# Performance work log

Hardware: AMD Instinct MI355X
Metric: run time of the kernel (lower is better)

The kernel has to match this reference:

```python
import jax, jax.numpy as jnp
import numpy as np

B, T, NIN, H1, H2, E, A = 256, 128, 1024, 512, 512, 256, 16
EPS = 1e-5


def setup_inputs() -> dict:
    key = jax.random.key(0)
    ks = jax.random.split(key, 24)
    def lin(k, fan_in, fan_out):
        # weights stored [in, out]; y = x @ W + b (equivalent to torch Linear)
        s = 1.0 / np.sqrt(fan_in)
        kw, kb = jax.random.split(k)
        return (jax.random.uniform(kw, (fan_in, fan_out), jnp.float32, -s, s),
                jax.random.uniform(kb, (fan_out,), jnp.float32, -s, s))
    W1, b1 = lin(ks[0], NIN, H1)
    W2, b2 = lin(ks[1], H1, H2)
    W3, b3 = lin(ks[2], H2, E)
    Wih, bih = lin(ks[3], E, 3 * E)   # GRUCell input weights, gate order [r, z, n]
    Whh, bhh = lin(ks[4], E, 3 * E)   # GRUCell hidden weights
    Whe, bhe = lin(ks[5], E + A, E)   # hidden_encoder
    Wae, bae = lin(ks[6], A, A)       # action_encoder
    return {
        'obs': jax.random.normal(ks[7], (B, T, NIN), jnp.float32),
        'actions': jax.random.normal(ks[8], (B, T, A), jnp.float32),
        'W1': W1, 'b1': b1, 'g1': jnp.ones((H1,), jnp.float32), 'be1': jnp.zeros((H1,), jnp.float32),
        'W2': W2, 'b2': b2, 'g2': jnp.ones((H2,), jnp.float32), 'be2': jnp.zeros((H2,), jnp.float32),
        'W3': W3, 'b3': b3,
        'Wih': Wih, 'bih': bih, 'Whh': Whh, 'bhh': bhh,
        'Whe': Whe, 'bhe': bhe, 'Wae': Wae, 'bae': bae,
    }


def reference(obs, actions, W1, b1, g1, be1, W2, b2, g2, be2, W3, b3,
              Wih, bih, Whh, bhh, Whe, bhe, Wae, bae):
    def bn(x, g, b):  # BatchNorm1d, training mode (batch stats, biased var)
        mu = jnp.mean(x, axis=0)
        var = jnp.mean((x - mu) ** 2, axis=0)
        return g * (x - mu) / jnp.sqrt(var + EPS) + b

    def mlp(x):
        x = jax.nn.elu(bn(x @ W1 + b1, g1, be1))
        x = jax.nn.elu(bn(x @ W2 + b2, g2, be2))
        return x @ W3 + b3

    def gru(x, h):
        gi = x @ Wih + bih
        gh = h @ Whh + bhh
        ir, iz, inn = jnp.split(gi, 3, axis=1)
        hr, hz, hn = jnp.split(gh, 3, axis=1)
        r = jax.nn.sigmoid(ir + hr)
        z = jax.nn.sigmoid(iz + hz)
        n = jnp.tanh(inn + r * hn)
        return (1.0 - z) * n + z * h

    obs_t = jnp.swapaxes(obs, 0, 1)       # [T, B, NIN]
    act_t = jnp.swapaxes(actions, 0, 1)   # [T, B, A]
    h0 = jnp.zeros((obs.shape[0], E), jnp.float32)
    a0 = jnp.zeros((obs.shape[0], A), jnp.float32)

    def step(carry, xs):
        h, a_prev = carry
        o, a = xs
        h = jnp.concatenate([h, a_prev], axis=1) @ Whe + bhe
        a_prev = a @ Wae + bae
        h = gru(mlp(o), h)
        return (h, a_prev), None

    (h, _), _ = jax.lax.scan(step, (h0, a0), (obs_t, act_t))
    return h
```

## Files before the change

kernel.cpp:

```cpp
#include <hip/hip_runtime.h>
#include <math.h>
#include <stdint.h>

#define B_   256
#define T_   128
#define NIN_ 1024
#define H1_  512
#define E_   256
#define A_   16
#define MT_  (B_ * T_)

typedef unsigned short ushort_t;
typedef unsigned long long ull_t;
typedef __attribute__((ext_vector_type(8))) short   short8;
typedef __attribute__((ext_vector_type(8))) __bf16  bf16x8;
typedef __attribute__((ext_vector_type(4))) float   f32x4;

union frag8 { short8 s; bf16x8 b; };

__device__ __forceinline__ ushort_t f2bf(float f) {
  union { float f; unsigned u; } v; v.f = f;
  unsigned r = (v.u + 0x7FFFu + ((v.u >> 16) & 1u)) >> 16;
  return (ushort_t)r;
}

static constexpr size_t OFF_C0    = 0;
static constexpr size_t OFF_OBSB  = 0;
static constexpr size_t OFF_Y     = 134217728;
static constexpr size_t OFF_YG    = 134217728;
static constexpr size_t OFF_XG    = 167772160;
static constexpr size_t OFF_PENCB = 184549376;
static constexpr size_t OFF_XB    = 201326592;
static constexpr size_t OFF_INN   = 201326592;
static constexpr size_t OFF_AE    = 234881024;
static constexpr size_t OFF_W1T   = 236978176;
static constexpr size_t OFF_W2T   = 238026752;
static constexpr size_t OFF_W3T   = 238551040;
static constexpr size_t OFF_WIHT  = 239075328;
static constexpr size_t OFF_WHHT  = 239468544;
static constexpr size_t OFF_WCT   = 240123904;
static constexpr size_t OFF_BSUM  = 241172480;
static constexpr size_t OFF_FLAGS = 241176576;
static constexpr size_t OFF_HG    = 241238016;


__global__ __launch_bounds__(256) void cast_obs_k(const float* __restrict__ obs,
                                                  ushort_t* __restrict__ out) {
  int row_in = blockIdx.x;
  int b = row_in / T_, t = row_in - b * T_;
  const float4* s4 = (const float4*)(obs + (size_t)row_in * NIN_);
  float4 v = s4[threadIdx.x];
  ushort_t* d = out + (size_t)(t * B_ + b) * NIN_ + threadIdx.x * 4;
  d[0] = f2bf(v.x); d[1] = f2bf(v.y); d[2] = f2bf(v.z); d[3] = f2bf(v.w);
}

__global__ __launch_bounds__(256) void transpose_cast_k(const float* __restrict__ in,
                                                        ushort_t* __restrict__ out,
                                                        int R, int C) {
  __shared__ float tile[32][33];
  int c0 = blockIdx.x * 32, r0 = blockIdx.y * 32;
  int tx = threadIdx.x & 31, ty = threadIdx.x >> 5;
  for (int i = 0; i < 4; i++) {
    int r = r0 + ty * 4 + i;
    if (r < R && (c0 + tx) < C) tile[ty * 4 + i][tx] = in[(size_t)r * C + c0 + tx];
  }
  __syncthreads();
  for (int i = 0; i < 4; i++) {
    int c = c0 + ty * 4 + i, r = r0 + tx;
    if (c < C && r < R) out[(size_t)c * R + r] = f2bf(tile[tx][ty * 4 + i]);
  }
}

__global__ __launch_bounds__(256) void wct_a_k(const float* __restrict__ Whe,
                                               ushort_t* __restrict__ Wct) {
  int c = blockIdx.x, k = threadIdx.x;
  Wct[(size_t)c * 256 + k] = f2bf(Whe[(size_t)k * 256 + c]);
}

__global__ __launch_bounds__(256) void wct_b_k(const float* __restrict__ Whe,
                                               const float* __restrict__ Whh,
                                               ushort_t* __restrict__ Wct) {
  int c = blockIdx.x;
  int k = threadIdx.x;
  float acc = 0.f;
  for (int j = 0; j < 256; j++)
    acc += Whe[(size_t)k * 256 + j] * Whh[(size_t)j * 768 + c];
  Wct[(size_t)(256 + c) * 256 + k] = f2bf(acc);
}

__global__ void bsum_k(const float* __restrict__ bih, const float* __restrict__ bhh,
                       float* __restrict__ bs) {
  int i = blockIdx.x * 256 + threadIdx.x;
  if (i < 768) bs[i] = bih[i] + bhh[i];
}

__global__ void init_flags_k(unsigned* f) {
  if (threadIdx.x < 16) f[threadIdx.x * 32] = 0u;
}

__global__ __launch_bounds__(256) void ae_k(const float* __restrict__ actions,
                                            const float* __restrict__ Wae,
                                            const float* __restrict__ bae,
                                            float* __restrict__ AE) {
  int idx = blockIdx.x * 256 + threadIdx.x;
  int m = idx >> 4, k2 = idx & 15;
  int t = m >> 8, b = m & 255;
  const float* arow = actions + ((size_t)b * T_ + t) * A_;
  float acc = bae[k2];
  for (int k = 0; k < 16; k++) acc += arow[k] * Wae[k * 16 + k2];
  AE[(size_t)m * 16 + k2] = acc;
}

__global__ __launch_bounds__(256) void penc_k(const float* __restrict__ AE,
                                              const float* __restrict__ Whe,
                                              const float* __restrict__ bhe,
                                              float* __restrict__ C0,
                                              ushort_t* __restrict__ Pencb) {
  int m = blockIdx.x;
  int j = threadIdx.x;
  __shared__ float a[16];
  if (threadIdx.x < 16)
    a[threadIdx.x] = (m >= B_) ? AE[(size_t)(m - B_) * 16 + threadIdx.x] : 0.f;
  __syncthreads();
  float acc = bhe[j];
  if (m >= B_) {
    for (int k = 0; k < 16; k++) acc += a[k] * Whe[(size_t)(256 + k) * 256 + j];
  }
  C0[(size_t)m * 1024 + j] = acc;
  Pencb[(size_t)m * 256 + j] = f2bf(acc);
}

__global__ __launch_bounds__(256) void bn_elu_k(const float* __restrict__ Y,
                                                const float* __restrict__ g,
                                                const float* __restrict__ be,
                                                ushort_t* __restrict__ Xb) {
  int t = blockIdx.x, f = blockIdx.y * 256 + threadIdx.x;
  const float* base = Y + (size_t)t * B_ * H1_;
  float s = 0.f, ss = 0.f;
  for (int b = 0; b < B_; b++) {
    float v = base[(size_t)b * H1_ + f];
    s += v; ss += v * v;
  }
  float mu  = s * (1.f / B_);
  float var = ss * (1.f / B_) - mu * mu;
  float inv = 1.f / sqrtf(var + 1e-5f);
  float sc = g[f] * inv, sh = be[f] - mu * sc;
  ushort_t* ob = Xb + (size_t)t * B_ * H1_;
  for (int b = 0; b < B_; b++) {
    float v = base[(size_t)b * H1_ + f] * sc + sh;
    float e = v > 0.f ? v : (expf(v) - 1.f);
    ob[(size_t)b * H1_ + f] = f2bf(e);
  }
}

__global__ __launch_bounds__(256) void cast_k(const float* __restrict__ in,
                                              ushort_t* __restrict__ out, long n) {
  long i = (long)blockIdx.x * 256 + threadIdx.x;
  if (i < n) out[i] = f2bf(in[i]);
}

__global__ __launch_bounds__(256) void gemm_bt_k(const ushort_t* __restrict__ A, int lda,
                                                 const ushort_t* __restrict__ Bt, int ldb,
                                                 float* __restrict__ C, int ldc,
                                                 const float* __restrict__ bias,
                                                 int K, int accum) {
  __shared__ __align__(16) ushort_t As[128][40];
  __shared__ __align__(16) ushort_t Bs[128][40];
  int tid = threadIdx.x;
  int wave = tid >> 6, lane = tid & 63;
  int q = lane >> 4, l15 = lane & 15;
  int wr = wave >> 1, wc = wave & 1;
  int m0 = blockIdx.x * 128, n0 = blockIdx.y * 128;
  f32x4 acc[4][4] = {};
  int r = tid >> 1, sh = (tid & 1) * 16;
  const ushort_t* aSrc = A + (size_t)(m0 + r) * lda + sh;
  const ushort_t* bSrc = Bt + (size_t)(n0 + r) * ldb + sh;
  for (int k0 = 0; k0 < K; k0 += 32) {
    *(short8*)&As[r][sh]     = *(const short8*)(aSrc + k0);
    *(short8*)&As[r][sh + 8] = *(const short8*)(aSrc + k0 + 8);
    *(short8*)&Bs[r][sh]     = *(const short8*)(bSrc + k0);
    *(short8*)&Bs[r][sh + 8] = *(const short8*)(bSrc + k0 + 8);
    __syncthreads();
    frag8 af[4], bf[4];
#pragma unroll
    for (int i = 0; i < 4; i++) {
      af[i].s = *(const short8*)&As[wr * 64 + i * 16 + l15][q * 8];
      bf[i].s = *(const short8*)&Bs[wc * 64 + i * 16 + l15][q * 8];
    }
#pragma unroll
    for (int at = 0; at < 4; at++)
#pragma unroll
      for (int bt = 0; bt < 4; bt++)
        acc[at][bt] = __builtin_amdgcn_mfma_f32_16x16x32_bf16(af[at].b, bf[bt].b, acc[at][bt], 0, 0, 0);
    __syncthreads();
  }
#pragma unroll
  for (int at = 0; at < 4; at++)
#pragma unroll
    for (int bt = 0; bt < 4; bt++) {
      int mb = m0 + wr * 64 + at * 16 + q * 4;
      int n  = n0 + wc * 64 + bt * 16 + l15;
      float bv = bias ? bias[n] : 0.f;
#pragma unroll
      for (int i = 0; i < 4; i++) {
        size_t idx = (size_t)(mb + i) * ldc + n;
        float v = acc[at][bt][i] + bv;
        if (accum) v += C[idx];
        C[idx] = v;
      }
    }
}

__global__ __launch_bounds__(1024) void gru_cols_k(
    const ushort_t* __restrict__ Wct,
    const float* __restrict__ C0,
    const float* __restrict__ INN,
    ull_t* __restrict__ hG,
    unsigned* __restrict__ flags,
    float* __restrict__ outF) {
  __shared__ __align__(16) ushort_t Wb[256][264];
  __shared__ __align__(16) ushort_t h_lds[16][264];
  __shared__ float G[4][16][66];
  __shared__ unsigned go, lcnt;

  const int tid = threadIdx.x;
  const int w = tid >> 6, lane = tid & 63;
  const int q = lane >> 4, l15 = lane & 15;
  const int rg = blockIdx.x & 15, cg = blockIdx.x >> 4;
  const int r0 = rg * 16;
  const int g = w >> 2, j = w & 3;

  unsigned* flag = flags + rg * 32;

  if (tid == 0) { go = 0u; lcnt = 0u; }
  for (int d = tid; d < 16 * 264 / 2; d += 1024) ((unsigned*)h_lds)[d] = 0u;
  for (int i = tid; i < 256 * 32; i += 1024) {
    int rr = i >> 5, ss = i & 31;
    int srow = (rr >> 6) * 256 + cg * 64 + (rr & 63);
    *(short8*)&Wb[rr][ss * 8] = *(const short8*)(Wct + (size_t)srow * 256 + ss * 8);
  }
  __syncthreads();

  const int crow = w;
  const int ccol = lane;
  const int hg = cg * 64 + ccol;

  for (int t = 0; t < T_; t++) {
    const float* c0t  = C0  + ((size_t)t * B_ + r0) * 1024;
    const float* innt = INN + ((size_t)t * B_ + r0) * 256;
    float c0he = c0t[(size_t)crow * 1024 + hg];
    float c0r  = c0t[(size_t)crow * 1024 + 256 + hg];
    float c0z  = c0t[(size_t)crow * 1024 + 512 + hg];
    float c0hn = c0t[(size_t)crow * 1024 + 768 + hg];
    float c0in = innt[(size_t)crow * 256 + hg];

    if (t > 0) {
      if (w == 0) {
        if (lane == 0) {
          while (__hip_atomic_load(flag, __ATOMIC_ACQUIRE, __HIP_MEMORY_SCOPE_AGENT) < 4u * (unsigned)t)
            __builtin_amdgcn_s_sleep(2);
          __hip_atomic_store(&go, (unsigned)t, __ATOMIC_RELEASE, __HIP_MEMORY_SCOPE_WORKGROUP);
        }
      } else {
        if (lane == 0) {
          while (__hip_atomic_load(&go, __ATOMIC_ACQUIRE, __HIP_MEMORY_SCOPE_WORKGROUP) < (unsigned)t)
            __builtin_amdgcn_s_sleep(1);
        }
      }
      if (tid < 768) {
        int s = tid >> 8;
        int cgs = s + (s >= cg ? 1 : 0);
        int rem = tid & 255;
        int row = rem >> 4, cp = rem & 15;
        ull_t v = __hip_atomic_load(&hG[(size_t)(t & 1) * 256 * 64 + (size_t)(r0 + row) * 64 + cgs * 16 + cp],
                                    __ATOMIC_RELAXED, __HIP_MEMORY_SCOPE_AGENT);
        *(ull_t*)&h_lds[row][cgs * 64 + cp * 4] = v;
      }
      __syncthreads();
    }

    f32x4 acc = {};
#pragma unroll
    for (int kc = 0; kc < 8; kc++) {
      frag8 a, b;
      a.s = *(const short8*)&h_lds[l15][kc * 32 + q * 8];
      b.s = *(const short8*)&Wb[g * 64 + j * 16 + l15][kc * 32 + q * 8];
      acc = __builtin_amdgcn_mfma_f32_16x16x32_bf16(a.b, b.b, acc, 0, 0, 0);
    }
#pragma unroll
    for (int i = 0; i < 4; i++) G[g][q * 4 + i][j * 16 + l15] = acc[i];
    __syncthreads();

    float henc = G[0][crow][ccol] + c0he;
    float rp   = G[1][crow][ccol] + c0r;
    float zp   = G[2][crow][ccol] + c0z;
    float hn   = G[3][crow][ccol] + c0hn;
    float rgate = 1.f / (1.f + expf(-rp));
    float zgate = 1.f / (1.f + expf(-zp));
    float ng = tanhf(c0in + rgate * hn);
    float hv = (1.f - zgate) * ng + zgate * henc;

    if (t < T_ - 1) {
      unsigned hvb = (unsigned)f2bf(hv);
      h_lds[crow][cg * 64 + ccol] = (ushort_t)hvb;
      unsigned p1 = (unsigned)__shfl_xor((int)hvb, 1);
      unsigned v32 = hvb | (p1 << 16);
      unsigned p2 = (unsigned)__shfl_xor((int)v32, 2);
      if ((lane & 3) == 0) {
        ull_t v64 = (ull_t)v32 | ((ull_t)p2 << 32);
        __hip_atomic_store(&hG[(size_t)((t + 1) & 1) * 256 * 64 + (size_t)(r0 + crow) * 64 + cg * 16 + (lane >> 2)],
                           v64, __ATOMIC_RELAXED, __HIP_MEMORY_SCOPE_AGENT);
      }
      asm volatile("s_waitcnt vmcnt(0)" ::: "memory");
      if (lane == 0) {
        unsigned old = __hip_atomic_fetch_add(&lcnt, 1u, __ATOMIC_ACQ_REL, __HIP_MEMORY_SCOPE_WORKGROUP);
        if (old == 16u * (unsigned)t + 15u)
          __hip_atomic_fetch_add(flag, 1u, __ATOMIC_RELEASE, __HIP_MEMORY_SCOPE_AGENT);
      }
    } else {
      outF[(size_t)(r0 + crow) * 256 + hg] = hv;
    }
  }
}

extern "C" void kernel_launch(void* const* d_in, const int* in_sizes, int n_in,
                              void* d_out, int out_size, void* d_ws, size_t ws_size,
                              hipStream_t stream) {
  const float* obs     = (const float*)d_in[0];
  const float* actions = (const float*)d_in[1];
  const float* W1  = (const float*)d_in[2];
  const float* b1  = (const float*)d_in[3];
  const float* g1  = (const float*)d_in[4];
  const float* be1 = (const float*)d_in[5];
  const float* W2  = (const float*)d_in[6];
  const float* b2  = (const float*)d_in[7];
  const float* g2  = (const float*)d_in[8];
  const float* be2 = (const float*)d_in[9];
  const float* W3  = (const float*)d_in[10];
  const float* b3  = (const float*)d_in[11];
  const float* Wih = (const float*)d_in[12];
  const float* bih = (const float*)d_in[13];
  const float* Whh = (const float*)d_in[14];
  const float* bhh = (const float*)d_in[15];
  const float* Whe = (const float*)d_in[16];
  const float* bhe = (const float*)d_in[17];
  const float* Wae = (const float*)d_in[18];
  const float* bae = (const float*)d_in[19];

  char* ws = (char*)d_ws;
  float*    C0    = (float*)(ws + OFF_C0);
  ushort_t* obsb  = (ushort_t*)(ws + OFF_OBSB);
  float*    Y     = (float*)(ws + OFF_Y);
  float*    Yg    = (float*)(ws + OFF_YG);
  ushort_t* XG    = (ushort_t*)(ws + OFF_XG);
  ushort_t* Pencb = (ushort_t*)(ws + OFF_PENCB);
  ushort_t* Xb    = (ushort_t*)(ws + OFF_XB);
  float*    INN   = (float*)(ws + OFF_INN);
  float*    AE    = (float*)(ws + OFF_AE);
  ushort_t* W1t   = (ushort_t*)(ws + OFF_W1T);
  ushort_t* W2t   = (ushort_t*)(ws + OFF_W2T);
  ushort_t* W3t   = (ushort_t*)(ws + OFF_W3T);
  ushort_t* Wiht  = (ushort_t*)(ws + OFF_WIHT);
  ushort_t* Whht  = (ushort_t*)(ws + OFF_WHHT);
  ushort_t* Wct   = (ushort_t*)(ws + OFF_WCT);
  float*    bsum  = (float*)(ws + OFF_BSUM);
  unsigned* flags = (unsigned*)(ws + OFF_FLAGS);
  ull_t*    hG    = (ull_t*)(ws + OFF_HG);
  float*    outF  = (float*)d_out;

  cast_obs_k<<<MT_, 256, 0, stream>>>(obs, obsb);
  transpose_cast_k<<<dim3(16, 32), 256, 0, stream>>>(W1, W1t, 1024, 512);
  transpose_cast_k<<<dim3(16, 16), 256, 0, stream>>>(W2, W2t, 512, 512);
  transpose_cast_k<<<dim3(8, 16),  256, 0, stream>>>(W3, W3t, 512, 256);
  transpose_cast_k<<<dim3(24, 8),  256, 0, stream>>>(Wih, Wiht, 256, 768);
  transpose_cast_k<<<dim3(24, 8),  256, 0, stream>>>(Whh, Whht, 256, 768);
  wct_a_k<<<256, 256, 0, stream>>>(Whe, Wct);
  wct_b_k<<<768, 256, 0, stream>>>(Whe, Whh, Wct);
  bsum_k<<<3, 256, 0, stream>>>(bih, bhh, bsum);
  init_flags_k<<<1, 64, 0, stream>>>(flags);
  ae_k<<<MT_ * 16 / 256, 256, 0, stream>>>(actions, Wae, bae, AE);

  gemm_bt_k<<<dim3(256, 4), 256, 0, stream>>>(obsb, 1024, W1t, 1024, Y, 512, b1, 1024, 0);
  bn_elu_k<<<dim3(T_, 2), 256, 0, stream>>>(Y, g1, be1, Xb);
  gemm_bt_k<<<dim3(256, 4), 256, 0, stream>>>(Xb, 512, W2t, 512, Y, 512, b2, 512, 0);
  bn_elu_k<<<dim3(T_, 2), 256, 0, stream>>>(Y, g2, be2, Xb);
  gemm_bt_k<<<dim3(256, 2), 256, 0, stream>>>(Xb, 512, W3t, 512, Yg, 256, b3, 512, 0);
  cast_k<<<MT_ * 256 / 256, 256, 0, stream>>>(Yg, XG, (long)MT_ * 256);

  penc_k<<<MT_, 256, 0, stream>>>(AE, Whe, bhe, C0, Pencb);
  gemm_bt_k<<<dim3(256, 4), 256, 0, stream>>>(XG, 256, Wiht, 256, C0 + 256, 1024, bsum, 256, 0);
  gemm_bt_k<<<dim3(256, 4), 256, 0, stream>>>(Pencb, 256, Whht, 256, C0 + 256, 1024, nullptr, 256, 1);
  gemm_bt_k<<<dim3(256, 2), 256, 0, stream>>>(Pencb, 256, Whht + 512 * 256, 256, C0 + 768, 1024, bhh + 512, 256, 0);
  gemm_bt_k<<<dim3(256, 2), 256, 0, stream>>>(XG, 256, Wiht + 512 * 256, 256, INN, 256, bih + 512, 256, 0);

  gru_cols_k<<<64, 1024, 0, stream>>>(Wct, C0, INN, hG, flags, outF);
}
```

Measured before the change: 1.283 ms.

## Concatenate GRU gate inputs into K=512 GEMM and simplify recurrent-kernel sync

The third MLP GEMM now writes bf16 directly into a combined [x | penc] buffer, which removes the separate fp32-to-bf16 cast kernel. The r/z gate projections of input and hidden are merged into one GEMM with K=512 over concatenated weights, replacing two GEMMs and an accumulate pass. In the recurrent kernel, the two-level flag/LDS spin handshake is replaced by a single thread polling plus __syncthreads, and h is staged through LDS before 64-bit global stores. The extra block-wide barriers per step may add latency on the serial critical path.

After: 1.115 ms. 1.15x faster.

```diff
diff --git a/kernel.cpp b/kernel.cpp
--- a/kernel.cpp
+++ b/kernel.cpp
@@ -27,17 +27,14 @@
 static constexpr size_t OFF_C0    = 0;
 static constexpr size_t OFF_OBSB  = 0;
 static constexpr size_t OFF_Y     = 134217728;
-static constexpr size_t OFF_YG    = 134217728;
-static constexpr size_t OFF_XG    = 167772160;
-static constexpr size_t OFF_PENCB = 184549376;
+static constexpr size_t OFF_XGP   = 167772160;
 static constexpr size_t OFF_XB    = 201326592;
 static constexpr size_t OFF_INN   = 201326592;
 static constexpr size_t OFF_AE    = 234881024;
 static constexpr size_t OFF_W1T   = 236978176;
 static constexpr size_t OFF_W2T   = 238026752;
 static constexpr size_t OFF_W3T   = 238551040;
-static constexpr size_t OFF_WIHT  = 239075328;
-static constexpr size_t OFF_WHHT  = 239468544;
+static constexpr size_t OFF_WC    = 239075328;
 static constexpr size_t OFF_WCT   = 240123904;
 static constexpr size_t OFF_BSUM  = 241172480;
 static constexpr size_t OFF_FLAGS = 241176576;
@@ -56,7 +53,7 @@
 
 __global__ __launch_bounds__(256) void transpose_cast_k(const float* __restrict__ in,
                                                         ushort_t* __restrict__ out,
-                                                        int R, int C) {
+                                                        int R, int C, int ldo) {
   __shared__ float tile[32][33];
   int c0 = blockIdx.x * 32, r0 = blockIdx.y * 32;
   int tx = threadIdx.x & 31, ty = threadIdx.x >> 5;
@@ -67,7 +64,7 @@
   __syncthreads();
   for (int i = 0; i < 4; i++) {
     int c = c0 + ty * 4 + i, r = r0 + tx;
-    if (c < C && r < R) out[(size_t)c * R + r] = f2bf(tile[tx][ty * 4 + i]);
+    if (c < C && r < R) out[(size_t)c * ldo + r] = f2bf(tile[tx][ty * 4 + i]);
   }
 }
 
@@ -115,7 +112,7 @@
                                               const float* __restrict__ Whe,
                                               const float* __restrict__ bhe,
                                               float* __restrict__ C0,
-                                              ushort_t* __restrict__ Pencb) {
+                                              ushort_t* __restrict__ XGP) {
   int m = blockIdx.x;
   int j = threadIdx.x;
   __shared__ float a[16];
@@ -127,7 +124,7 @@
     for (int k = 0; k < 16; k++) acc += a[k] * Whe[(size_t)(256 + k) * 256 + j];
   }
   C0[(size_t)m * 1024 + j] = acc;
-  Pencb[(size_t)m * 256 + j] = f2bf(acc);
+  XGP[(size_t)m * 512 + 256 + j] = f2bf(acc);
 }
 
 __global__ __launch_bounds__(256) void bn_elu_k(const float* __restrict__ Y,
@@ -153,15 +150,10 @@
   }
 }
 
-__global__ __launch_bounds__(256) void cast_k(const float* __restrict__ in,
-                                              ushort_t* __restrict__ out, long n) {
-  long i = (long)blockIdx.x * 256 + threadIdx.x;
-  if (i < n) out[i] = f2bf(in[i]);
-}
-
 __global__ __launch_bounds__(256) void gemm_bt_k(const ushort_t* __restrict__ A, int lda,
                                                  const ushort_t* __restrict__ Bt, int ldb,
-                                                 float* __restrict__ C, int ldc,
+                                                 float* __restrict__ C,
+                                                 ushort_t* __restrict__ Cb, int ldc,
                                                  const float* __restrict__ bias,
                                                  int K, int accum) {
   __shared__ __align__(16) ushort_t As[128][40];
@@ -205,8 +197,12 @@
       for (int i = 0; i < 4; i++) {
         size_t idx = (size_t)(mb + i) * ldc + n;
         float v = acc[at][bt][i] + bv;
-        if (accum) v += C[idx];
-        C[idx] = v;
+        if (Cb) {
+          Cb[idx] = f2bf(v);
+        } else {
+          if (accum) v += C[idx];
+          C[idx] = v;
+        }
       }
     }
 }
@@ -221,7 +217,6 @@
   __shared__ __align__(16) ushort_t Wb[256][264];
   __shared__ __align__(16) ushort_t h_lds[16][264];
   __shared__ float G[4][16][66];
-  __shared__ unsigned go, lcnt;
 
   const int tid = threadIdx.x;
   const int w = tid >> 6, lane = tid & 63;
@@ -232,7 +227,6 @@
 
   unsigned* flag = flags + rg * 32;
 
-  if (tid == 0) { go = 0u; lcnt = 0u; }
   for (int d = tid; d < 16 * 264 / 2; d += 1024) ((unsigned*)h_lds)[d] = 0u;
   for (int i = tid; i < 256 * 32; i += 1024) {
     int rr = i >> 5, ss = i & 31;
@@ -255,18 +249,12 @@
     float c0in = innt[(size_t)crow * 256 + hg];
 
     if (t > 0) {
-      if (w == 0) {
-        if (lane == 0) {
-          while (__hip_atomic_load(flag, __ATOMIC_ACQUIRE, __HIP_MEMORY_SCOPE_AGENT) < 4u * (unsigned)t)
-            __builtin_amdgcn_s_sleep(2);
-          __hip_atomic_store(&go, (unsigned)t, __ATOMIC_RELEASE, __HIP_MEMORY_SCOPE_WORKGROUP);
-        }
-      } else {
-        if (lane == 0) {
-          while (__hip_atomic_load(&go, __ATOMIC_ACQUIRE, __HIP_MEMORY_SCOPE_WORKGROUP) < (unsigned)t)
-            __builtin_amdgcn_s_sleep(1);
-        }
+      if (tid == 0) {
+        unsigned target = 4u * (unsigned)t;
+        while (__hip_atomic_load(flag, __ATOMIC_ACQUIRE, __HIP_MEMORY_SCOPE_AGENT) < target)
+          __builtin_amdgcn_s_sleep(1);
       }
+      __syncthreads();
       if (tid < 768) {
         int s = tid >> 8;
         int cgs = s + (s >= cg ? 1 : 0);
@@ -301,22 +289,17 @@
     float hv = (1.f - zgate) * ng + zgate * henc;
 
     if (t < T_ - 1) {
-      unsigned hvb = (unsigned)f2bf(hv);
-      h_lds[crow][cg * 64 + ccol] = (ushort_t)hvb;
-      unsigned p1 = (unsigned)__shfl_xor((int)hvb, 1);
-      unsigned v32 = hvb | (p1 << 16);
-      unsigned p2 = (unsigned)__shfl_xor((int)v32, 2);
-      if ((lane & 3) == 0) {
-        ull_t v64 = (ull_t)v32 | ((ull_t)p2 << 32);
-        __hip_atomic_store(&hG[(size_t)((t + 1) & 1) * 256 * 64 + (size_t)(r0 + crow) * 64 + cg * 16 + (lane >> 2)],
-                           v64, __ATOMIC_RELAXED, __HIP_MEMORY_SCOPE_AGENT);
+      h_lds[crow][cg * 64 + ccol] = f2bf(hv);
+      __syncthreads();
+      if (tid < 256) {
+        int row2 = tid >> 4, cp = tid & 15;
+        ull_t v = *(const ull_t*)&h_lds[row2][cg * 64 + cp * 4];
+        __hip_atomic_store(&hG[(size_t)((t + 1) & 1) * 256 * 64 + (size_t)(r0 + row2) * 64 + cg * 16 + cp],
+                           v, __ATOMIC_RELAXED, __HIP_MEMORY_SCOPE_AGENT);
       }
-      asm volatile("s_waitcnt vmcnt(0)" ::: "memory");
-      if (lane == 0) {
-        unsigned old = __hip_atomic_fetch_add(&lcnt, 1u, __ATOMIC_ACQ_REL, __HIP_MEMORY_SCOPE_WORKGROUP);
-        if (old == 16u * (unsigned)t + 15u)
-          __hip_atomic_fetch_add(flag, 1u, __ATOMIC_RELEASE, __HIP_MEMORY_SCOPE_AGENT);
-      }
+      __syncthreads();
+      if (tid == 0)
+        __hip_atomic_fetch_add(flag, 1u, __ATOMIC_RELEASE, __HIP_MEMORY_SCOPE_AGENT);
     } else {
       outF[(size_t)(r0 + crow) * 256 + hg] = hv;
     }
@@ -351,17 +334,14 @@
   float*    C0    = (float*)(ws + OFF_C0);
   ushort_t* obsb  = (ushort_t*)(ws + OFF_OBSB);
   float*    Y     = (float*)(ws + OFF_Y);
-  float*    Yg    = (float*)(ws + OFF_YG);
-  ushort_t* XG    = (ushort_t*)(ws + OFF_XG);
-  ushort_t* Pencb = (ushort_t*)(ws + OFF_PENCB);
+  ushort_t* XGP   = (ushort_t*)(ws + OFF_XGP);
   ushort_t* Xb    = (ushort_t*)(ws + OFF_XB);
   float*    INN   = (float*)(ws + OFF_INN);
   float*    AE    = (float*)(ws + OFF_AE);
   ushort_t* W1t   = (ushort_t*)(ws + OFF_W1T);
   ushort_t* W2t   = (ushort_t*)(ws + OFF_W2T);
   ushort_t* W3t   = (ushort_t*)(ws + OFF_W3T);
-  ushort_t* Wiht  = (ushort_t*)(ws + OFF_WIHT);
-  ushort_t* Whht  = (ushort_t*)(ws + OFF_WHHT);
+  ushort_t* WC    = (ushort_t*)(ws + OFF_WC);
   ushort_t* Wct   = (ushort_t*)(ws + OFF_WCT);
   float*    bsum  = (float*)(ws + OFF_BSUM);
   unsigned* flags = (unsigned*)(ws + OFF_FLAGS);
@@ -369,29 +349,27 @@
   float*    outF  = (float*)d_out;
 
   cast_obs_k<<<MT_, 256, 0, stream>>>(obs, obsb);
-  transpose_cast_k<<<dim3(16, 32), 256, 0, stream>>>(W1, W1t, 1024, 512);
-  transpose_cast_k<<<dim3(16, 16), 256, 0, stream>>>(W2, W2t, 512, 512);
-  transpose_cast_k<<<dim3(8, 16),  256, 0, stream>>>(W3, W3t, 512, 256);
-  transpose_cast_k<<<dim3(24, 8),  256, 0, stream>>>(Wih, Wiht, 256, 768);
-  transpose_cast_k<<<dim3(24, 8),  256, 0, stream>>>(Whh, Whht, 256, 768);
+  transpose_cast_k<<<dim3(16, 32), 256, 0, stream>>>(W1, W1t, 1024, 512, 1024);
+  transpose_cast_k<<<dim3(16, 16), 256, 0, stream>>>(W2, W2t, 512, 512, 512);
+  transpose_cast_k<<<dim3(8, 16),  256, 0, stream>>>(W3, W3t, 512, 256, 512);
+  transpose_cast_k<<<dim3(24, 8),  256, 0, stream>>>(Wih, WC, 256, 768, 512);
+  transpose_cast_k<<<dim3(24, 8),  256, 0, stream>>>(Whh, WC + 256, 256, 768, 512);
   wct_a_k<<<256, 256, 0, stream>>>(Whe, Wct);
   wct_b_k<<<768, 256, 0, stream>>>(Whe, Whh, Wct);
   bsum_k<<<3, 256, 0, stream>>>(bih, bhh, bsum);
   init_flags_k<<<1, 64, 0, stream>>>(flags);
   ae_k<<<MT_ * 16 / 256, 256, 0, stream>>>(actions, Wae, bae, AE);
 
-  gemm_bt_k<<<dim3(256, 4), 256, 0, stream>>>(obsb, 1024, W1t, 1024, Y, 512, b1, 1024, 0);
+  gemm_bt_k<<<dim3(256, 4), 256, 0, stream>>>(obsb, 1024, W1t, 1024, Y, nullptr, 512, b1, 1024, 0);
   bn_elu_k<<<dim3(T_, 2), 256, 0, stream>>>(Y, g1, be1, Xb);
-  gemm_bt_k<<<dim3(256, 4), 256, 0, stream>>>(Xb, 512, W2t, 512, Y, 512, b2, 512, 0);
+  gemm_bt_k<<<dim3(256, 4), 256, 0, stream>>>(Xb, 512, W2t, 512, Y, nullptr, 512, b2, 512, 0);
   bn_elu_k<<<dim3(T_, 2), 256, 0, stream>>>(Y, g2, be2, Xb);
-  gemm_bt_k<<<dim3(256, 2), 256, 0, stream>>>(Xb, 512, W3t, 512, Yg, 256, b3, 512, 0);
-  cast_k<<<MT_ * 256 / 256, 256, 0, stream>>>(Yg, XG, (long)MT_ * 256);
-
-  penc_k<<<MT_, 256, 0, stream>>>(AE, Whe, bhe, C0, Pencb);
-  gemm_bt_k<<<dim3(256, 4), 256, 0, stream>>>(XG, 256, Wiht, 256, C0 + 256, 1024, bsum, 256, 0);
-  gemm_bt_k<<<dim3(256, 4), 256, 0, stream>>>(Pencb, 256, Whht, 256, C0 + 256, 1024, nullptr, 256, 1);
-  gemm_bt_k<<<dim3(256, 2), 256, 0, stream>>>(Pencb, 256, Whht + 512 * 256, 256, C0 + 768, 1024, bhh + 512, 256, 0);
-  gemm_bt_k<<<dim3(256, 2), 256, 0, stream>>>(XG, 256, Wiht + 512 * 256, 256, INN, 256, bih + 512, 256, 0);
+  gemm_bt_k<<<dim3(256, 2), 256, 0, stream>>>(Xb, 512, W3t, 512, nullptr, XGP, 512, b3, 512, 0);
+
+  penc_k<<<MT_, 256, 0, stream>>>(AE, Whe, bhe, C0, XGP);
+  gemm_bt_k<<<dim3(256, 4), 256, 0, stream>>>(XGP, 512, WC, 512, C0 + 256, nullptr, 1024, bsum, 512, 0);
+  gemm_bt_k<<<dim3(256, 2), 256, 0, stream>>>(XGP + 256, 512, WC + 512 * 512 + 256, 512, C0 + 768, nullptr, 1024, bhh + 512, 256, 0);
+  gemm_bt_k<<<dim3(256, 2), 256, 0, stream>>>(XGP, 512, WC + 512 * 512, 512, INN, nullptr, 256, bih + 512, 256, 0);
 
   gru_cols_k<<<64, 1024, 0, stream>>>(Wct, C0, INN, hG, flags, outF);
 }
```
